# Optimization experiments

Hardware: AMD Instinct MI355X
Metric: run time of the kernel (lower is better)

Reference implementation:

```python
import jax, jax.numpy as jnp
import numpy as np

N_NODES = 100000
N_EDGES = 1600000
D_FEAT = 64  # node feature dim; apply_func indim = 2*D_FEAT, outdim = D_FEAT


def setup_inputs() -> dict:
    key = jax.random.key(0)
    k1, k2, k3, k4 = jax.random.split(key, 4)
    h = jax.random.normal(k1, (N_NODES, D_FEAT), dtype=jnp.float32)
    src = jax.random.randint(k2, (N_EDGES,), 0, N_NODES, dtype=jnp.int32)
    dst = jax.random.randint(k3, (N_EDGES,), 0, N_NODES, dtype=jnp.int32)
    W = jax.random.normal(k4, (D_FEAT, 2 * D_FEAT), dtype=jnp.float32) / jnp.sqrt(2.0 * D_FEAT)
    b = jnp.zeros((D_FEAT,), dtype=jnp.float32)
    return {"h": h, "W": W, "b": b, "src": src, "dst": dst}


def reference(h, W, b, src, dst):
    n = h.shape[0]
    # message passing: gather source features, mean-reduce per destination node
    msgs = h[src]                                                # [E, D]
    summed = jax.ops.segment_sum(msgs, dst, num_segments=n)     # [N, D]
    deg = jax.ops.segment_sum(jnp.ones(dst.shape, h.dtype), dst, num_segments=n)  # [N]
    c = summed / jnp.maximum(deg, 1.0)[:, None]                 # mean aggregate
    # update: concat(h, c) -> linear -> L2 normalize -> relu
    bundle = jnp.concatenate([h, c], axis=1) @ W.T + b           # [N, D]
    norm = jnp.linalg.norm(bundle, axis=1, keepdims=True)
    bundle = bundle / jnp.maximum(norm, 1e-12)                   # F.normalize(p=2, dim=1)
    new_h = jax.nn.relu(bundle)
    # DGL update_all only touches nodes that received messages
    h_upd = jnp.where(deg[:, None] > 0, new_h, h)
    # residual (indim == outdim)
    return h + h_upd
```

## Files before the change

### kernel.cpp

```cpp
#include <hip/hip_runtime.h>

#define DF 64
#define ELLK 32
#define NB 1024
#define BSTR 1792
#define NPB 98

typedef __attribute__((ext_vector_type(8))) short bf16x8;
typedef __attribute__((ext_vector_type(4))) float f32x4;

__device__ __forceinline__ unsigned short bf16rne(float f) {
    unsigned u = __float_as_uint(f);
    unsigned r = u + 0x7fffu + ((u >> 16) & 1u);
    return (unsigned short)(r >> 16);
}
__device__ __forceinline__ float b2f(unsigned short u) {
    return __uint_as_float((unsigned)u << 16);
}

__global__ __launch_bounds__(256) void conv_zero(
    const float* __restrict__ h, unsigned short* __restrict__ hbs,
    int* __restrict__ gcur, int* __restrict__ ovfcnt, int N)
{
    int tid = blockIdx.x * 256 + threadIdx.x;
    if (tid < NB) gcur[tid] = 0;
    if (tid == NB) *ovfcnt = 0;
    if (tid < (N + 1) * 8) {
        int n = tid >> 3, f8 = tid & 7;
        unsigned short* op = &hbs[(size_t)n * DF + f8 * 8];
        if (n == N) {
            ushort4 z = {0, 0, 0, 0};
            *(ushort4*)op = z; *(ushort4*)(op + 4) = z;
        } else {
            const float* hp = &h[(size_t)n * DF + f8 * 8];
            float4 v0 = *(const float4*)hp;
            float4 v1 = *(const float4*)(hp + 4);
            ushort4 o0, o1;
            o0.x = bf16rne(v0.x); o0.y = bf16rne(v0.y); o0.z = bf16rne(v0.z); o0.w = bf16rne(v0.w);
            o1.x = bf16rne(v1.x); o1.y = bf16rne(v1.y); o1.z = bf16rne(v1.z); o1.w = bf16rne(v1.w);
            *(ushort4*)op = o0;
            *(ushort4*)(op + 4) = o1;
        }
    }
}

#define EPT 13
__global__ __launch_bounds__(256) void bin_edges(
    const int* __restrict__ src, const int* __restrict__ dst,
    int* __restrict__ gcur, unsigned* __restrict__ pairs,
    int* __restrict__ ovf, int* __restrict__ ovfcnt, int ovfcap, int E, int N)
{
    __shared__ unsigned hist[NB];
    __shared__ unsigned base_s[NB];
    int t = threadIdx.x;
    for (int i = t; i < NB; i += 256) hist[i] = 0;
    __syncthreads();

    int e0 = blockIdx.x * (EPT * 256);
    unsigned pk[EPT];
    #pragma unroll
    for (int k = 0; k < EPT; ++k) {
        int e = e0 + k * 256 + t;
        pk[k] = 0xFFFFFFFFu;
        if (e < E) {
            int d = dst[e];
            unsigned bkt = (unsigned)(((unsigned long long)d * NB) / (unsigned)N);
            unsigned r = atomicAdd(&hist[bkt], 1u);
            pk[k] = (r << 10) | bkt;
        }
    }
    __syncthreads();
    int rot = (blockIdx.x * 67) & (NB - 1);
    for (int i = t; i < NB; i += 256) {
        int ii = (i + rot) & (NB - 1);
        unsigned hv = hist[ii];
        if (hv) base_s[ii] = (unsigned)atomicAdd(&gcur[ii], (int)hv);
    }
    __syncthreads();

    #pragma unroll
    for (int k = 0; k < EPT; ++k) {
        if (pk[k] != 0xFFFFFFFFu) {
            int e = e0 + k * 256 + t;
            int d = dst[e], s = src[e];
            unsigned bkt = pk[k] & (NB - 1u);
            unsigned pos = base_s[bkt] + (pk[k] >> 10);
            if (pos < BSTR) {
                int lo = (int)(((long long)bkt * N + NB - 1) / NB);
                pairs[(size_t)bkt * BSTR + pos] = ((unsigned)(d - lo) << 17) | (unsigned)s;
            } else {
                int p = atomicAdd(ovfcnt, 1);
                if (p < ovfcap) { ovf[2 * p] = d; ovf[2 * p + 1] = s; }
            }
        }
    }
}

__global__ __launch_bounds__(512) void build_gather(
    const unsigned* __restrict__ pairs, const int* __restrict__ gcur,
    const unsigned short* __restrict__ hbs,
    int* __restrict__ cnt, unsigned short* __restrict__ csum,
    int* __restrict__ ovf, int* __restrict__ ovfcnt, int ovfcap, int N)
{
    __shared__ int ell_l[NPB * ELLK];
    __shared__ int cnt_l[NPB];
    int b = blockIdx.x, t = threadIdx.x;
    int lo = (int)(((long long)b * N + NB - 1) / NB);
    int hi = (int)(((long long)(b + 1) * N + NB - 1) / NB);
    if (hi > N) hi = N;
    int nn = hi - lo;
    for (int i = t; i < nn; i += 512) cnt_l[i] = 0;
    __syncthreads();

    int count = gcur[b]; if (count > BSTR) count = BSTR;
    const unsigned* pb = &pairs[(size_t)b * BSTR];
    for (int i = t; i < count; i += 512) {
        unsigned p = pb[i];
        int ld = (int)(p >> 17);
        int s  = (int)(p & 131071u);
        int slot = atomicAdd(&cnt_l[ld], 1);
        if (slot < ELLK) {
            ell_l[ld * ELLK + (((slot & 7) << 2) | (slot >> 3))] = s;
        } else {
            int q = atomicAdd(ovfcnt, 1);
            if (q < ovfcap) { ovf[2 * q] = lo + ld; ovf[2 * q + 1] = s; }
        }
    }
    __syncthreads();

    const int lane = t & 63, wv = t >> 6;
    const int ew = lane >> 3;
    const int f8 = lane & 7;

    for (int ld = wv; ld < nn; ld += 8) {
        int cv = cnt_l[ld];
        int m = cv < ELLK ? cv : ELLK;
        int ms = __builtin_amdgcn_readfirstlane(m);
        int4 pv = ((const int4*)&ell_l[ld * ELLK])[ew];

        int i0 = (ew     < m) ? pv.x : N;
        int i1 = (ew + 8 < m) ? pv.y : N;
        bf16x8 v0 = *(const bf16x8*)&hbs[(size_t)i0 * DF + f8 * 8];
        bf16x8 v1 = *(const bf16x8*)&hbs[(size_t)i1 * DF + f8 * 8];
        bf16x8 v2 = {0,0,0,0,0,0,0,0};
        bf16x8 v3 = {0,0,0,0,0,0,0,0};
        if (ms > 16) {
            int i2 = (ew + 16 < m) ? pv.z : N;
            v2 = *(const bf16x8*)&hbs[(size_t)i2 * DF + f8 * 8];
            if (ms > 24) {
                int i3 = (ew + 24 < m) ? pv.w : N;
                v3 = *(const bf16x8*)&hbs[(size_t)i3 * DF + f8 * 8];
            }
        }

        float a[8];
        #pragma unroll
        for (int j = 0; j < 8; ++j)
            a[j] = (b2f((unsigned short)v0[j]) + b2f((unsigned short)v1[j]))
                 + (b2f((unsigned short)v2[j]) + b2f((unsigned short)v3[j]));

        #pragma unroll
        for (int msk = 8; msk <= 32; msk <<= 1) {
            #pragma unroll
            for (int j = 0; j < 8; ++j) a[j] += __shfl_xor(a[j], msk);
        }

        if (ew == 0) {
            bf16x8 o;
            #pragma unroll
            for (int j = 0; j < 8; ++j) o[j] = (short)bf16rne(a[j]);
            *(bf16x8*)&csum[(size_t)(lo + ld) * DF + f8 * 8] = o;
        }
    }

    for (int i = t; i < nn; i += 512) {
        int c = cnt_l[i];
        cnt[lo + i] = c < ELLK ? c : ELLK;
    }
}

__global__ __launch_bounds__(256) void sage_update_mfma(
    const float* __restrict__ h, const float* __restrict__ W,
    const float* __restrict__ b, const int* __restrict__ cnt,
    const unsigned short* __restrict__ hbs,
    const unsigned short* __restrict__ csum,
    const int* __restrict__ ovf, const int* __restrict__ ovfcnt,
    int ovfcap, float* __restrict__ out, int N)
{
    const int lane = threadIdx.x & 63;
    const int wave = threadIdx.x >> 6;
    const int c = lane & 15;
    const int q = lane >> 4;

    bf16x8 bf[4][4];
    #pragma unroll
    for (int nt = 0; nt < 4; ++nt) {
        #pragma unroll
        for (int kt = 0; kt < 4; ++kt) {
            const float* wp = &W[(size_t)(nt * 16 + c) * 128 + kt * 32 + q * 8];
            float4 w0 = *(const float4*)wp;
            float4 w1 = *(const float4*)(wp + 4);
            bf16x8 f;
            f[0] = (short)bf16rne(w0.x); f[1] = (short)bf16rne(w0.y);
            f[2] = (short)bf16rne(w0.z); f[3] = (short)bf16rne(w0.w);
            f[4] = (short)bf16rne(w1.x); f[5] = (short)bf16rne(w1.y);
            f[6] = (short)bf16rne(w1.z); f[7] = (short)bf16rne(w1.w);
            bf[nt][kt] = f;
        }
    }
    float bias[4];
    #pragma unroll
    for (int nt = 0; nt < 4; ++nt) bias[nt] = b[nt * 16 + c];

    int oc = *ovfcnt; if (oc > ovfcap) oc = ovfcap;

    int gwave = blockIdx.x * 4 + wave;
    int nwave = gridDim.x * 4;
    int ntiles = (N + 15) >> 4;

    for (int tile = gwave; tile < ntiles; tile += nwave) {
        int n0 = tile << 4;
        int nm = n0 + c;
        int nmc = nm < N ? nm : N - 1;
        int deg = cnt[nmc];
        int extra = 0;
        if (oc > 0) {
            for (int t = 0; t < oc; ++t)
                if (ovf[2 * t] == nm) extra++;
        }
        int dtot = deg + extra;
        float inv = 1.0f / fmaxf((float)dtot, 1.0f);

        bf16x8 a0 = *(const bf16x8*)&hbs[(size_t)nmc * DF + q * 8];
        bf16x8 a1 = *(const bf16x8*)&hbs[(size_t)nmc * DF + 32 + q * 8];
        bf16x8 a2, a3;
        #pragma unroll
        for (int kc = 0; kc < 2; ++kc) {
            bf16x8 u = *(const bf16x8*)&csum[(size_t)nmc * DF + kc * 32 + q * 8];
            float e[8];
            #pragma unroll
            for (int i = 0; i < 8; ++i) e[i] = b2f((unsigned short)u[i]);
            if (oc > 0) {
                for (int t = 0; t < oc; ++t) {
                    if (ovf[2 * t] == nm) {
                        bf16x8 hu = *(const bf16x8*)&hbs[(size_t)ovf[2 * t + 1] * DF + kc * 32 + q * 8];
                        #pragma unroll
                        for (int i = 0; i < 8; ++i) e[i] += b2f((unsigned short)hu[i]);
                    }
                }
            }
            bf16x8 f;
            #pragma unroll
            for (int i = 0; i < 8; ++i) f[i] = (short)bf16rne(e[i] * inv);
            if (kc == 0) a2 = f; else a3 = f;
        }

        f32x4 acc0 = {bias[0], bias[0], bias[0], bias[0]};
        f32x4 acc1 = {bias[1], bias[1], bias[1], bias[1]};
        f32x4 acc2 = {bias[2], bias[2], bias[2], bias[2]};
        f32x4 acc3 = {bias[3], bias[3], bias[3], bias[3]};
        acc0 = __builtin_amdgcn_mfma_f32_16x16x32_bf16(a0, bf[0][0], acc0, 0, 0, 0);
        acc0 = __builtin_amdgcn_mfma_f32_16x16x32_bf16(a1, bf[0][1], acc0, 0, 0, 0);
        acc0 = __builtin_amdgcn_mfma_f32_16x16x32_bf16(a2, bf[0][2], acc0, 0, 0, 0);
        acc0 = __builtin_amdgcn_mfma_f32_16x16x32_bf16(a3, bf[0][3], acc0, 0, 0, 0);
        acc1 = __builtin_amdgcn_mfma_f32_16x16x32_bf16(a0, bf[1][0], acc1, 0, 0, 0);
        acc1 = __builtin_amdgcn_mfma_f32_16x16x32_bf16(a1, bf[1][1], acc1, 0, 0, 0);
        acc1 = __builtin_amdgcn_mfma_f32_16x16x32_bf16(a2, bf[1][2], acc1, 0, 0, 0);
        acc1 = __builtin_amdgcn_mfma_f32_16x16x32_bf16(a3, bf[1][3], acc1, 0, 0, 0);
        acc2 = __builtin_amdgcn_mfma_f32_16x16x32_bf16(a0, bf[2][0], acc2, 0, 0, 0);
        acc2 = __builtin_amdgcn_mfma_f32_16x16x32_bf16(a1, bf[2][1], acc2, 0, 0, 0);
        acc2 = __builtin_amdgcn_mfma_f32_16x16x32_bf16(a2, bf[2][2], acc2, 0, 0, 0);
        acc2 = __builtin_amdgcn_mfma_f32_16x16x32_bf16(a3, bf[2][3], acc2, 0, 0, 0);
        acc3 = __builtin_amdgcn_mfma_f32_16x16x32_bf16(a0, bf[3][0], acc3, 0, 0, 0);
        acc3 = __builtin_amdgcn_mfma_f32_16x16x32_bf16(a1, bf[3][1], acc3, 0, 0, 0);
        acc3 = __builtin_amdgcn_mfma_f32_16x16x32_bf16(a2, bf[3][2], acc3, 0, 0, 0);
        acc3 = __builtin_amdgcn_mfma_f32_16x16x32_bf16(a3, bf[3][3], acc3, 0, 0, 0);

        float ss[4];
        #pragma unroll
        for (int r = 0; r < 4; ++r)
            ss[r] = acc0[r] * acc0[r] + acc1[r] * acc1[r]
                  + acc2[r] * acc2[r] + acc3[r] * acc3[r];
        #pragma unroll
        for (int msk = 1; msk <= 8; msk <<= 1) {
            ss[0] += __shfl_xor(ss[0], msk);
            ss[1] += __shfl_xor(ss[1], msk);
            ss[2] += __shfl_xor(ss[2], msk);
            ss[3] += __shfl_xor(ss[3], msk);
        }
        #pragma unroll
        for (int r = 0; r < 4; ++r) {
            int nr = n0 + q * 4 + r;
            int dr = __shfl(deg + extra, q * 4 + r);
            if (nr < N) {
                float rin = 1.0f / fmaxf(sqrtf(ss[r]), 1e-12f);
                const float* hp = &h[(size_t)nr * DF + c];
                float hv0 = hp[0], hv1 = hp[16], hv2 = hp[32], hv3 = hp[48];
                bool up = dr > 0;
                float o0 = hv0 + (up ? fmaxf(acc0[r] * rin, 0.f) : hv0);
                float o1 = hv1 + (up ? fmaxf(acc1[r] * rin, 0.f) : hv1);
                float o2 = hv2 + (up ? fmaxf(acc2[r] * rin, 0.f) : hv2);
                float o3 = hv3 + (up ? fmaxf(acc3[r] * rin, 0.f) : hv3);
                float* op = &out[(size_t)nr * DF + c];
                op[0] = o0; op[16] = o1; op[32] = o2; op[48] = o3;
            }
        }
    }
}

extern "C" void kernel_launch(void* const* d_in, const int* in_sizes, int n_in,
                              void* d_out, int out_size, void* d_ws, size_t ws_size,
                              hipStream_t stream) {
    const float* h   = (const float*)d_in[0];
    const float* W   = (const float*)d_in[1];
    const float* b   = (const float*)d_in[2];
    const int*   src = (const int*)d_in[3];
    const int*   dst = (const int*)d_in[4];
    float* out = (float*)d_out;

    const int N = in_sizes[0] / DF;
    const int E = in_sizes[3];

    int* cnt    = (int*)d_ws;
    int* ovfcnt = cnt + N;
    int* gcur   = cnt + ((N + 31) & ~15);
    unsigned short* hbs  = (unsigned short*)(gcur + ((NB + 15) & ~15));
    unsigned short* csum = hbs + (((size_t)(N + 1) * DF + 15) & ~(size_t)15);
    unsigned* pairs = (unsigned*)(csum + (((size_t)N * DF + 15) & ~(size_t)15));
    int* ovf    = (int*)(pairs + (size_t)NB * BSTR);
    size_t used = (size_t)((char*)ovf - (char*)d_ws);
    int ovfcap  = (ws_size > used + 64) ? (int)((ws_size - used) / 8 - 4) : 0;

    conv_zero<<<((N + 1) * 8 + 255) / 256, 256, 0, stream>>>(h, hbs, gcur, ovfcnt, N);

    bin_edges<<<(E + EPT * 256 - 1) / (EPT * 256), 256, 0, stream>>>(
        src, dst, gcur, pairs, ovf, ovfcnt, ovfcap, E, N);

    build_gather<<<NB, 512, 0, stream>>>(
        pairs, gcur, hbs, cnt, csum, ovf, ovfcnt, ovfcap, N);

    sage_update_mfma<<<512, 256, 0, stream>>>(
        h, W, b, cnt, hbs, csum, ovf, ovfcnt, ovfcap, out, N);
}
```

Baseline: 207.5 us.

## Use coarser 256-bucket binning with four gather blocks per bucket

```diff
diff --git a/kernel.cpp b/kernel.cpp
--- a/kernel.cpp
+++ b/kernel.cpp
@@ -2,8 +2,9 @@
 
 #define DF 64
 #define ELLK 32
-#define NB 1024
-#define BSTR 1792
+#define NBB 256
+#define GQ 4
+#define BSTR 7168
 #define NPB 98
 
 typedef __attribute__((ext_vector_type(8))) short bf16x8;
@@ -23,8 +24,8 @@
     int* __restrict__ gcur, int* __restrict__ ovfcnt, int N)
 {
     int tid = blockIdx.x * 256 + threadIdx.x;
-    if (tid < NB) gcur[tid] = 0;
-    if (tid == NB) *ovfcnt = 0;
+    if (tid < NBB) gcur[tid] = 0;
+    if (tid == NBB) *ovfcnt = 0;
     if (tid < (N + 1) * 8) {
         int n = tid >> 3, f8 = tid & 7;
         unsigned short* op = &hbs[(size_t)n * DF + f8 * 8];
@@ -50,10 +51,10 @@
     int* __restrict__ gcur, unsigned* __restrict__ pairs,
     int* __restrict__ ovf, int* __restrict__ ovfcnt, int ovfcap, int E, int N)
 {
-    __shared__ unsigned hist[NB];
-    __shared__ unsigned base_s[NB];
+    __shared__ unsigned hist[NBB];
+    __shared__ unsigned base_s[NBB];
     int t = threadIdx.x;
-    for (int i = t; i < NB; i += 256) hist[i] = 0;
+    if (t < NBB) hist[t] = 0;
     __syncthreads();
 
     int e0 = blockIdx.x * (EPT * 256);
@@ -64,15 +65,15 @@
         pk[k] = 0xFFFFFFFFu;
         if (e < E) {
             int d = dst[e];
-            unsigned bkt = (unsigned)(((unsigned long long)d * NB) / (unsigned)N);
+            unsigned bkt = (unsigned)(((unsigned long long)d * NBB) / (unsigned)N);
             unsigned r = atomicAdd(&hist[bkt], 1u);
-            pk[k] = (r << 10) | bkt;
-        }
-    }
-    __syncthreads();
-    int rot = (blockIdx.x * 67) & (NB - 1);
-    for (int i = t; i < NB; i += 256) {
-        int ii = (i + rot) & (NB - 1);
+            pk[k] = (r << 8) | bkt;
+        }
+    }
+    __syncthreads();
+    int rot = (blockIdx.x * 67) & (NBB - 1);
+    if (t < NBB) {
+        int ii = (t + rot) & (NBB - 1);
         unsigned hv = hist[ii];
         if (hv) base_s[ii] = (unsigned)atomicAdd(&gcur[ii], (int)hv);
     }
@@ -83,10 +84,10 @@
         if (pk[k] != 0xFFFFFFFFu) {
             int e = e0 + k * 256 + t;
             int d = dst[e], s = src[e];
-            unsigned bkt = pk[k] & (NB - 1u);
-            unsigned pos = base_s[bkt] + (pk[k] >> 10);
+            unsigned bkt = pk[k] & (NBB - 1u);
+            unsigned pos = base_s[bkt] + (pk[k] >> 8);
             if (pos < BSTR) {
-                int lo = (int)(((long long)bkt * N + NB - 1) / NB);
+                int lo = (int)(((long long)bkt * N + NBB - 1) / NBB);
                 pairs[(size_t)bkt * BSTR + pos] = ((unsigned)(d - lo) << 17) | (unsigned)s;
             } else {
                 int p = atomicAdd(ovfcnt, 1);
@@ -104,26 +105,34 @@
 {
     __shared__ int ell_l[NPB * ELLK];
     __shared__ int cnt_l[NPB];
-    int b = blockIdx.x, t = threadIdx.x;
-    int lo = (int)(((long long)b * N + NB - 1) / NB);
-    int hi = (int)(((long long)(b + 1) * N + NB - 1) / NB);
-    if (hi > N) hi = N;
-    int nn = hi - lo;
-    for (int i = t; i < nn; i += 512) cnt_l[i] = 0;
+    int b = blockIdx.x >> 2, qt = blockIdx.x & 3;
+    int t = threadIdx.x;
+    int lo_b = (int)(((long long)b * N + NBB - 1) / NBB);
+    int hi_b = (int)(((long long)(b + 1) * N + NBB - 1) / NBB);
+    if (hi_b > N) hi_b = N;
+    int nn_b = hi_b - lo_b;
+    int q0 = qt * NPB;
+    int qn = nn_b - q0; if (qn > NPB) qn = NPB;
+    if (qn <= 0) return;
+    int nbase = lo_b + q0;
+
+    for (int i = t; i < qn; i += 512) cnt_l[i] = 0;
     __syncthreads();
 
     int count = gcur[b]; if (count > BSTR) count = BSTR;
     const unsigned* pb = &pairs[(size_t)b * BSTR];
     for (int i = t; i < count; i += 512) {
         unsigned p = pb[i];
-        int ld = (int)(p >> 17);
-        int s  = (int)(p & 131071u);
-        int slot = atomicAdd(&cnt_l[ld], 1);
-        if (slot < ELLK) {
-            ell_l[ld * ELLK + (((slot & 7) << 2) | (slot >> 3))] = s;
-        } else {
-            int q = atomicAdd(ovfcnt, 1);
-            if (q < ovfcap) { ovf[2 * q] = lo + ld; ovf[2 * q + 1] = s; }
+        int ld = (int)(p >> 17) - q0;
+        if ((unsigned)ld < (unsigned)qn) {
+            int s = (int)(p & 131071u);
+            int slot = atomicAdd(&cnt_l[ld], 1);
+            if (slot < ELLK) {
+                ell_l[ld * ELLK + (((slot & 7) << 2) | (slot >> 3))] = s;
+            } else {
+                int q = atomicAdd(ovfcnt, 1);
+                if (q < ovfcap) { ovf[2 * q] = nbase + ld; ovf[2 * q + 1] = s; }
+            }
         }
     }
     __syncthreads();
@@ -132,7 +141,7 @@
     const int ew = lane >> 3;
     const int f8 = lane & 7;
 
-    for (int ld = wv; ld < nn; ld += 8) {
+    for (int ld = wv; ld < qn; ld += 8) {
         int cv = cnt_l[ld];
         int m = cv < ELLK ? cv : ELLK;
         int ms = __builtin_amdgcn_readfirstlane(m);
@@ -169,13 +178,13 @@
             bf16x8 o;
             #pragma unroll
             for (int j = 0; j < 8; ++j) o[j] = (short)bf16rne(a[j]);
-            *(bf16x8*)&csum[(size_t)(lo + ld) * DF + f8 * 8] = o;
-        }
-    }
-
-    for (int i = t; i < nn; i += 512) {
+            *(bf16x8*)&csum[(size_t)(nbase + ld) * DF + f8 * 8] = o;
+        }
+    }
+
+    for (int i = t; i < qn; i += 512) {
         int c = cnt_l[i];
-        cnt[lo + i] = c < ELLK ? c : ELLK;
+        cnt[nbase + i] = c < ELLK ? c : ELLK;
     }
 }
 
@@ -324,10 +333,10 @@
     int* cnt    = (int*)d_ws;
     int* ovfcnt = cnt + N;
     int* gcur   = cnt + ((N + 31) & ~15);
-    unsigned short* hbs  = (unsigned short*)(gcur + ((NB + 15) & ~15));
+    unsigned short* hbs  = (unsigned short*)(gcur + ((NBB + 15) & ~15));
     unsigned short* csum = hbs + (((size_t)(N + 1) * DF + 15) & ~(size_t)15);
     unsigned* pairs = (unsigned*)(csum + (((size_t)N * DF + 15) & ~(size_t)15));
-    int* ovf    = (int*)(pairs + (size_t)NB * BSTR);
+    int* ovf    = (int*)(pairs + (size_t)NBB * BSTR);
     size_t used = (size_t)((char*)ovf - (char*)d_ws);
     int ovfcap  = (ws_size > used + 64) ? (int)((ws_size - used) / 8 - 4) : 0;
 
@@ -336,7 +345,7 @@
     bin_edges<<<(E + EPT * 256 - 1) / (EPT * 256), 256, 0, stream>>>(
         src, dst, gcur, pairs, ovf, ovfcnt, ovfcap, E, N);
 
-    build_gather<<<NB, 512, 0, stream>>>(
+    build_gather<<<NBB * GQ, 512, 0, stream>>>(
         pairs, gcur, hbs, cnt, csum, ovf, ovfcnt, ovfcap, N);
 
     sage_update_mfma<<<512, 256, 0, stream>>>(
```

New measurement: 200.0 us. 3.6% less time.

## Scatter edges into a global ELL with atomics and fuse the gather into the update

Applied to the files above, without the earlier changes.

```diff
diff --git a/kernel.cpp b/kernel.cpp
--- a/kernel.cpp
+++ b/kernel.cpp
@@ -2,9 +2,8 @@
 
 #define DF 64
 #define ELLK 32
-#define NB 1024
-#define BSTR 1792
-#define NPB 98
+#define WIN 64
+#define CSTR 72
 
 typedef __attribute__((ext_vector_type(8))) short bf16x8;
 typedef __attribute__((ext_vector_type(4))) float f32x4;
@@ -18,13 +17,14 @@
     return __uint_as_float((unsigned)u << 16);
 }
 
-__global__ __launch_bounds__(256) void conv_zero(
-    const float* __restrict__ h, unsigned short* __restrict__ hbs,
-    int* __restrict__ gcur, int* __restrict__ ovfcnt, int N)
+__global__ __launch_bounds__(512) void conv_scatter(
+    const float* __restrict__ h, const int* __restrict__ src,
+    const int* __restrict__ dst, unsigned short* __restrict__ hbs,
+    int* __restrict__ cnt, int* __restrict__ ell,
+    int* __restrict__ ovf, int* __restrict__ ovfcnt, int ovfcap, int N, int E)
 {
-    int tid = blockIdx.x * 256 + threadIdx.x;
-    if (tid < NB) gcur[tid] = 0;
-    if (tid == NB) *ovfcnt = 0;
+    int tid = blockIdx.x * 512 + threadIdx.x;
+
     if (tid < (N + 1) * 8) {
         int n = tid >> 3, f8 = tid & 7;
         unsigned short* op = &hbs[(size_t)n * DF + f8 * 8];
@@ -42,156 +42,80 @@
             *(ushort4*)(op + 4) = o1;
         }
     }
-}
-
-#define EPT 13
-__global__ __launch_bounds__(256) void bin_edges(
-    const int* __restrict__ src, const int* __restrict__ dst,
-    int* __restrict__ gcur, unsigned* __restrict__ pairs,
-    int* __restrict__ ovf, int* __restrict__ ovfcnt, int ovfcap, int E, int N)
-{
-    __shared__ unsigned hist[NB];
-    __shared__ unsigned base_s[NB];
-    int t = threadIdx.x;
-    for (int i = t; i < NB; i += 256) hist[i] = 0;
-    __syncthreads();
-
-    int e0 = blockIdx.x * (EPT * 256);
-    unsigned pk[EPT];
-    #pragma unroll
-    for (int k = 0; k < EPT; ++k) {
-        int e = e0 + k * 256 + t;
-        pk[k] = 0xFFFFFFFFu;
-        if (e < E) {
-            int d = dst[e];
-            unsigned bkt = (unsigned)(((unsigned long long)d * NB) / (unsigned)N);
-            unsigned r = atomicAdd(&hist[bkt], 1u);
-            pk[k] = (r << 10) | bkt;
-        }
-    }
-    __syncthreads();
-    int rot = (blockIdx.x * 67) & (NB - 1);
-    for (int i = t; i < NB; i += 256) {
-        int ii = (i + rot) & (NB - 1);
-        unsigned hv = hist[ii];
-        if (hv) base_s[ii] = (unsigned)atomicAdd(&gcur[ii], (int)hv);
-    }
-    __syncthreads();
-
-    #pragma unroll
-    for (int k = 0; k < EPT; ++k) {
-        if (pk[k] != 0xFFFFFFFFu) {
-            int e = e0 + k * 256 + t;
-            int d = dst[e], s = src[e];
-            unsigned bkt = pk[k] & (NB - 1u);
-            unsigned pos = base_s[bkt] + (pk[k] >> 10);
-            if (pos < BSTR) {
-                int lo = (int)(((long long)bkt * N + NB - 1) / NB);
-                pairs[(size_t)bkt * BSTR + pos] = ((unsigned)(d - lo) << 17) | (unsigned)s;
-            } else {
-                int p = atomicAdd(ovfcnt, 1);
-                if (p < ovfcap) { ovf[2 * p] = d; ovf[2 * p + 1] = s; }
-            }
-        }
-    }
-}
-
-__global__ __launch_bounds__(512) void build_gather(
-    const unsigned* __restrict__ pairs, const int* __restrict__ gcur,
-    const unsigned short* __restrict__ hbs,
-    int* __restrict__ cnt, unsigned short* __restrict__ csum,
-    int* __restrict__ ovf, int* __restrict__ ovfcnt, int ovfcap, int N)
-{
-    __shared__ int ell_l[NPB * ELLK];
-    __shared__ int cnt_l[NPB];
-    int b = blockIdx.x, t = threadIdx.x;
-    int lo = (int)(((long long)b * N + NB - 1) / NB);
-    int hi = (int)(((long long)(b + 1) * N + NB - 1) / NB);
-    if (hi > N) hi = N;
-    int nn = hi - lo;
-    for (int i = t; i < nn; i += 512) cnt_l[i] = 0;
-    __syncthreads();
-
-    int count = gcur[b]; if (count > BSTR) count = BSTR;
-    const unsigned* pb = &pairs[(size_t)b * BSTR];
-    for (int i = t; i < count; i += 512) {
-        unsigned p = pb[i];
-        int ld = (int)(p >> 17);
-        int s  = (int)(p & 131071u);
-        int slot = atomicAdd(&cnt_l[ld], 1);
+
+    int stride = gridDim.x * 512;
+    for (int e = tid; e < E; e += stride) {
+        int d = dst[e], s = src[e];
+        int slot = atomicAdd(&cnt[d], 1);
         if (slot < ELLK) {
-            ell_l[ld * ELLK + (((slot & 7) << 2) | (slot >> 3))] = s;
+            ell[(size_t)d * ELLK + (((slot & 7) << 2) | (slot >> 3))] = s;
         } else {
-            int q = atomicAdd(ovfcnt, 1);
-            if (q < ovfcap) { ovf[2 * q] = lo + ld; ovf[2 * q + 1] = s; }
-        }
-    }
-    __syncthreads();
-
-    const int lane = t & 63, wv = t >> 6;
-    const int ew = lane >> 3;
-    const int f8 = lane & 7;
-
-    for (int ld = wv; ld < nn; ld += 8) {
-        int cv = cnt_l[ld];
-        int m = cv < ELLK ? cv : ELLK;
-        int ms = __builtin_amdgcn_readfirstlane(m);
-        int4 pv = ((const int4*)&ell_l[ld * ELLK])[ew];
-
-        int i0 = (ew     < m) ? pv.x : N;
-        int i1 = (ew + 8 < m) ? pv.y : N;
-        bf16x8 v0 = *(const bf16x8*)&hbs[(size_t)i0 * DF + f8 * 8];
-        bf16x8 v1 = *(const bf16x8*)&hbs[(size_t)i1 * DF + f8 * 8];
-        bf16x8 v2 = {0,0,0,0,0,0,0,0};
-        bf16x8 v3 = {0,0,0,0,0,0,0,0};
-        if (ms > 16) {
-            int i2 = (ew + 16 < m) ? pv.z : N;
-            v2 = *(const bf16x8*)&hbs[(size_t)i2 * DF + f8 * 8];
-            if (ms > 24) {
-                int i3 = (ew + 24 < m) ? pv.w : N;
-                v3 = *(const bf16x8*)&hbs[(size_t)i3 * DF + f8 * 8];
-            }
-        }
-
-        float a[8];
-        #pragma unroll
-        for (int j = 0; j < 8; ++j)
-            a[j] = (b2f((unsigned short)v0[j]) + b2f((unsigned short)v1[j]))
-                 + (b2f((unsigned short)v2[j]) + b2f((unsigned short)v3[j]));
-
-        #pragma unroll
-        for (int msk = 8; msk <= 32; msk <<= 1) {
-            #pragma unroll
-            for (int j = 0; j < 8; ++j) a[j] += __shfl_xor(a[j], msk);
-        }
-
-        if (ew == 0) {
-            bf16x8 o;
-            #pragma unroll
-            for (int j = 0; j < 8; ++j) o[j] = (short)bf16rne(a[j]);
-            *(bf16x8*)&csum[(size_t)(lo + ld) * DF + f8 * 8] = o;
-        }
-    }
-
-    for (int i = t; i < nn; i += 512) {
-        int c = cnt_l[i];
-        cnt[lo + i] = c < ELLK ? c : ELLK;
-    }
-}
-
-__global__ __launch_bounds__(256) void sage_update_mfma(
-    const float* __restrict__ h, const float* __restrict__ W,
-    const float* __restrict__ b, const int* __restrict__ cnt,
-    const unsigned short* __restrict__ hbs,
-    const unsigned short* __restrict__ csum,
+            int p = atomicAdd(ovfcnt, 1);
+            if (p < ovfcap) { ovf[2 * p] = d; ovf[2 * p + 1] = s; }
+        }
+    }
+}
+
+__global__ __launch_bounds__(256, 4) void gather_update(
+    const unsigned short* __restrict__ hbs, const int* __restrict__ cnt,
+    const int* __restrict__ ell, const float* __restrict__ h,
+    const float* __restrict__ W, const float* __restrict__ b,
     const int* __restrict__ ovf, const int* __restrict__ ovfcnt,
     int ovfcap, float* __restrict__ out, int N)
 {
-    const int lane = threadIdx.x & 63;
-    const int wave = threadIdx.x >> 6;
-    const int c = lane & 15;
-    const int q = lane >> 4;
-
+    __shared__ unsigned short csB[WIN * CSTR];
+    const int t = threadIdx.x, lane = t & 63, wv = t >> 6;
+    const int base = blockIdx.x * WIN;
+
+    const int ew = lane >> 3;
+    const int f8 = lane & 7;
+    for (int i = 0; i < WIN / 4; ++i) {
+        int ld = wv + 4 * i;
+        int n = base + ld;
+        if (n < N) {
+            int cv = cnt[n];
+            int m = cv < ELLK ? cv : ELLK;
+            int ms = __builtin_amdgcn_readfirstlane(m);
+            int4 pv = *(const int4*)&ell[(size_t)n * ELLK + 4 * ew];
+
+            int i0 = (ew     < m) ? pv.x : N;
+            int i1 = (ew + 8 < m) ? pv.y : N;
+            bf16x8 v0 = *(const bf16x8*)&hbs[(size_t)i0 * DF + f8 * 8];
+            bf16x8 v1 = *(const bf16x8*)&hbs[(size_t)i1 * DF + f8 * 8];
+            bf16x8 v2 = {0,0,0,0,0,0,0,0};
+            bf16x8 v3 = {0,0,0,0,0,0,0,0};
+            if (ms > 16) {
+                int i2 = (ew + 16 < m) ? pv.z : N;
+                v2 = *(const bf16x8*)&hbs[(size_t)i2 * DF + f8 * 8];
+                if (ms > 24) {
+                    int i3 = (ew + 24 < m) ? pv.w : N;
+                    v3 = *(const bf16x8*)&hbs[(size_t)i3 * DF + f8 * 8];
+                }
+            }
+
+            float a[8];
+            #pragma unroll
+            for (int j = 0; j < 8; ++j)
+                a[j] = (b2f((unsigned short)v0[j]) + b2f((unsigned short)v1[j]))
+                     + (b2f((unsigned short)v2[j]) + b2f((unsigned short)v3[j]));
+            #pragma unroll
+            for (int msk = 8; msk <= 32; msk <<= 1) {
+                #pragma unroll
+                for (int j = 0; j < 8; ++j) a[j] += __shfl_xor(a[j], msk);
+            }
+            if (ew == 0) {
+                bf16x8 o;
+                #pragma unroll
+                for (int j = 0; j < 8; ++j) o[j] = (short)bf16rne(a[j]);
+                *(bf16x8*)&csB[ld * CSTR + f8 * 8] = o;
+            }
+        } else if (ew == 0) {
+            bf16x8 z = {0,0,0,0,0,0,0,0};
+            *(bf16x8*)&csB[ld * CSTR + f8 * 8] = z;
+        }
+    }
+
+    const int c = lane & 15, q = lane >> 4;
     bf16x8 bf[4][4];
     #pragma unroll
     for (int nt = 0; nt < 4; ++nt) {
@@ -214,96 +138,86 @@
 
     int oc = *ovfcnt; if (oc > ovfcap) oc = ovfcap;
 
-    int gwave = blockIdx.x * 4 + wave;
-    int nwave = gridDim.x * 4;
-    int ntiles = (N + 15) >> 4;
-
-    for (int tile = gwave; tile < ntiles; tile += nwave) {
-        int n0 = tile << 4;
-        int nm = n0 + c;
-        int nmc = nm < N ? nm : N - 1;
-        int deg = cnt[nmc];
-        int extra = 0;
+    __syncthreads();
+
+    int wn0 = wv * 16;
+    int nm = base + wn0 + c;
+    int nmc = nm < N ? nm : N - 1;
+    int dtot = cnt[nmc];
+    float inv = 1.0f / fmaxf((float)dtot, 1.0f);
+
+    bf16x8 a0 = *(const bf16x8*)&hbs[(size_t)nmc * DF + q * 8];
+    bf16x8 a1 = *(const bf16x8*)&hbs[(size_t)nmc * DF + 32 + q * 8];
+    bf16x8 a2, a3;
+    #pragma unroll
+    for (int kc = 0; kc < 2; ++kc) {
+        bf16x8 u = *(const bf16x8*)&csB[(wn0 + c) * CSTR + kc * 32 + q * 8];
+        float e[8];
+        #pragma unroll
+        for (int i = 0; i < 8; ++i) e[i] = b2f((unsigned short)u[i]);
         if (oc > 0) {
-            for (int t = 0; t < oc; ++t)
-                if (ovf[2 * t] == nm) extra++;
-        }
-        int dtot = deg + extra;
-        float inv = 1.0f / fmaxf((float)dtot, 1.0f);
-
-        bf16x8 a0 = *(const bf16x8*)&hbs[(size_t)nmc * DF + q * 8];
-        bf16x8 a1 = *(const bf16x8*)&hbs[(size_t)nmc * DF + 32 + q * 8];
-        bf16x8 a2, a3;
+            for (int t2 = 0; t2 < oc; ++t2) {
+                if (ovf[2 * t2] == nm) {
+                    bf16x8 hu = *(const bf16x8*)&hbs[(size_t)ovf[2 * t2 + 1] * DF + kc * 32 + q * 8];
+                    #pragma unroll
+                    for (int i = 0; i < 8; ++i) e[i] += b2f((unsigned short)hu[i]);
+                }
+            }
+        }
+        bf16x8 f;
         #pragma unroll
-        for (int kc = 0; kc < 2; ++kc) {
-            bf16x8 u = *(const bf16x8*)&csum[(size_t)nmc * DF + kc * 32 + q * 8];
-            float e[8];
-            #pragma unroll
-            for (int i = 0; i < 8; ++i) e[i] = b2f((unsigned short)u[i]);
-            if (oc > 0) {
-                for (int t = 0; t < oc; ++t) {
-                    if (ovf[2 * t] == nm) {
-                        bf16x8 hu = *(const bf16x8*)&hbs[(size_t)ovf[2 * t + 1] * DF + kc * 32 + q * 8];
-                        #pragma unroll
-                        for (int i = 0; i < 8; ++i) e[i] += b2f((unsigned short)hu[i]);
-                    }
-                }
-            }
-            bf16x8 f;
-            #pragma unroll
-            for (int i = 0; i < 8; ++i) f[i] = (short)bf16rne(e[i] * inv);
-            if (kc == 0) a2 = f; else a3 = f;
-        }
-
-        f32x4 acc0 = {bias[0], bias[0], bias[0], bias[0]};
-        f32x4 acc1 = {bias[1], bias[1], bias[1], bias[1]};
-        f32x4 acc2 = {bias[2], bias[2], bias[2], bias[2]};
-        f32x4 acc3 = {bias[3], bias[3], bias[3], bias[3]};
-        acc0 = __builtin_amdgcn_mfma_f32_16x16x32_bf16(a0, bf[0][0], acc0, 0, 0, 0);
-        acc0 = __builtin_amdgcn_mfma_f32_16x16x32_bf16(a1, bf[0][1], acc0, 0, 0, 0);
-        acc0 = __builtin_amdgcn_mfma_f32_16x16x32_bf16(a2, bf[0][2], acc0, 0, 0, 0);
-        acc0 = __builtin_amdgcn_mfma_f32_16x16x32_bf16(a3, bf[0][3], acc0, 0, 0, 0);
-        acc1 = __builtin_amdgcn_mfma_f32_16x16x32_bf16(a0, bf[1][0], acc1, 0, 0, 0);
-        acc1 = __builtin_amdgcn_mfma_f32_16x16x32_bf16(a1, bf[1][1], acc1, 0, 0, 0);
-        acc1 = __builtin_amdgcn_mfma_f32_16x16x32_bf16(a2, bf[1][2], acc1, 0, 0, 0);
-        acc1 = __builtin_amdgcn_mfma_f32_16x16x32_bf16(a3, bf[1][3], acc1, 0, 0, 0);
-        acc2 = __builtin_amdgcn_mfma_f32_16x16x32_bf16(a0, bf[2][0], acc2, 0, 0, 0);
-        acc2 = __builtin_amdgcn_mfma_f32_16x16x32_bf16(a1, bf[2][1], acc2, 0, 0, 0);
-        acc2 = __builtin_amdgcn_mfma_f32_16x16x32_bf16(a2, bf[2][2], acc2, 0, 0, 0);
-        acc2 = __builtin_amdgcn_mfma_f32_16x16x32_bf16(a3, bf[2][3], acc2, 0, 0, 0);
-        acc3 = __builtin_amdgcn_mfma_f32_16x16x32_bf16(a0, bf[3][0], acc3, 0, 0, 0);
-        acc3 = __builtin_amdgcn_mfma_f32_16x16x32_bf16(a1, bf[3][1], acc3, 0, 0, 0);
-        acc3 = __builtin_amdgcn_mfma_f32_16x16x32_bf16(a2, bf[3][2], acc3, 0, 0, 0);
-        acc3 = __builtin_amdgcn_mfma_f32_16x16x32_bf16(a3, bf[3][3], acc3, 0, 0, 0);
-
-        float ss[4];
-        #pragma unroll
-        for (int r = 0; r < 4; ++r)
-            ss[r] = acc0[r] * acc0[r] + acc1[r] * acc1[r]
-                  + acc2[r] * acc2[r] + acc3[r] * acc3[r];
-        #pragma unroll
-        for (int msk = 1; msk <= 8; msk <<= 1) {
-            ss[0] += __shfl_xor(ss[0], msk);
-            ss[1] += __shfl_xor(ss[1], msk);
-            ss[2] += __shfl_xor(ss[2], msk);
-            ss[3] += __shfl_xor(ss[3], msk);
-        }
-        #pragma unroll
-        for (int r = 0; r < 4; ++r) {
-            int nr = n0 + q * 4 + r;
-            int dr = __shfl(deg + extra, q * 4 + r);
-            if (nr < N) {
-                float rin = 1.0f / fmaxf(sqrtf(ss[r]), 1e-12f);
-                const float* hp = &h[(size_t)nr * DF + c];
-                float hv0 = hp[0], hv1 = hp[16], hv2 = hp[32], hv3 = hp[48];
-                bool up = dr > 0;
-                float o0 = hv0 + (up ? fmaxf(acc0[r] * rin, 0.f) : hv0);
-                float o1 = hv1 + (up ? fmaxf(acc1[r] * rin, 0.f) : hv1);
-                float o2 = hv2 + (up ? fmaxf(acc2[r] * rin, 0.f) : hv2);
-                float o3 = hv3 + (up ? fmaxf(acc3[r] * rin, 0.f) : hv3);
-                float* op = &out[(size_t)nr * DF + c];
-                op[0] = o0; op[16] = o1; op[32] = o2; op[48] = o3;
-            }
+        for (int i = 0; i < 8; ++i) f[i] = (short)bf16rne(e[i] * inv);
+        if (kc == 0) a2 = f; else a3 = f;
+    }
+
+    f32x4 acc0 = {bias[0], bias[0], bias[0], bias[0]};
+    f32x4 acc1 = {bias[1], bias[1], bias[1], bias[1]};
+    f32x4 acc2 = {bias[2], bias[2], bias[2], bias[2]};
+    f32x4 acc3 = {bias[3], bias[3], bias[3], bias[3]};
+    acc0 = __builtin_amdgcn_mfma_f32_16x16x32_bf16(a0, bf[0][0], acc0, 0, 0, 0);
+    acc0 = __builtin_amdgcn_mfma_f32_16x16x32_bf16(a1, bf[0][1], acc0, 0, 0, 0);
+    acc0 = __builtin_amdgcn_mfma_f32_16x16x32_bf16(a2, bf[0][2], acc0, 0, 0, 0);
+    acc0 = __builtin_amdgcn_mfma_f32_16x16x32_bf16(a3, bf[0][3], acc0, 0, 0, 0);
+    acc1 = __builtin_amdgcn_mfma_f32_16x16x32_bf16(a0, bf[1][0], acc1, 0, 0, 0);
+    acc1 = __builtin_amdgcn_mfma_f32_16x16x32_bf16(a1, bf[1][1], acc1, 0, 0, 0);
+    acc1 = __builtin_amdgcn_mfma_f32_16x16x32_bf16(a2, bf[1][2], acc1, 0, 0, 0);
+    acc1 = __builtin_amdgcn_mfma_f32_16x16x32_bf16(a3, bf[1][3], acc1, 0, 0, 0);
+    acc2 = __builtin_amdgcn_mfma_f32_16x16x32_bf16(a0, bf[2][0], acc2, 0, 0, 0);
+    acc2 = __builtin_amdgcn_mfma_f32_16x16x32_bf16(a1, bf[2][1], acc2, 0, 0, 0);
+    acc2 = __builtin_amdgcn_mfma_f32_16x16x32_bf16(a2, bf[2][2], acc2, 0, 0, 0);
+    acc2 = __builtin_amdgcn_mfma_f32_16x16x32_bf16(a3, bf[2][3], acc2, 0, 0, 0);
+    acc3 = __builtin_amdgcn_mfma_f32_16x16x32_bf16(a0, bf[3][0], acc3, 0, 0, 0);
+    acc3 = __builtin_amdgcn_mfma_f32_16x16x32_bf16(a1, bf[3][1], acc3, 0, 0, 0);
+    acc3 = __builtin_amdgcn_mfma_f32_16x16x32_bf16(a2, bf[3][2], acc3, 0, 0, 0);
+    acc3 = __builtin_amdgcn_mfma_f32_16x16x32_bf16(a3, bf[3][3], acc3, 0, 0, 0);
+
+    float ss[4];
+    #pragma unroll
+    for (int r = 0; r < 4; ++r)
+        ss[r] = acc0[r] * acc0[r] + acc1[r] * acc1[r]
+              + acc2[r] * acc2[r] + acc3[r] * acc3[r];
+    #pragma unroll
+    for (int msk = 1; msk <= 8; msk <<= 1) {
+        ss[0] += __shfl_xor(ss[0], msk);
+        ss[1] += __shfl_xor(ss[1], msk);
+        ss[2] += __shfl_xor(ss[2], msk);
+        ss[3] += __shfl_xor(ss[3], msk);
+    }
+    #pragma unroll
+    for (int r = 0; r < 4; ++r) {
+        int nr = base + wn0 + q * 4 + r;
+        int dr = __shfl(dtot, q * 4 + r);
+        if (nr < N) {
+            float rin = 1.0f / fmaxf(sqrtf(ss[r]), 1e-12f);
+            const float* hp = &h[(size_t)nr * DF + c];
+            float hv0 = hp[0], hv1 = hp[16], hv2 = hp[32], hv3 = hp[48];
+            bool up = dr > 0;
+            float o0 = hv0 + (up ? fmaxf(acc0[r] * rin, 0.f) : hv0);
+            float o1 = hv1 + (up ? fmaxf(acc1[r] * rin, 0.f) : hv1);
+            float o2 = hv2 + (up ? fmaxf(acc2[r] * rin, 0.f) : hv2);
+            float o3 = hv3 + (up ? fmaxf(acc3[r] * rin, 0.f) : hv3);
+            float* op = &out[(size_t)nr * DF + c];
+            op[0] = o0; op[16] = o1; op[32] = o2; op[48] = o3;
         }
     }
 }
@@ -323,22 +237,17 @@
 
     int* cnt    = (int*)d_ws;
     int* ovfcnt = cnt + N;
-    int* gcur   = cnt + ((N + 31) & ~15);
-    unsigned short* hbs  = (unsigned short*)(gcur + ((NB + 15) & ~15));
-    unsigned short* csum = hbs + (((size_t)(N + 1) * DF + 15) & ~(size_t)15);
-    unsigned* pairs = (unsigned*)(csum + (((size_t)N * DF + 15) & ~(size_t)15));
-    int* ovf    = (int*)(pairs + (size_t)NB * BSTR);
+    int* ell    = cnt + ((N + 1 + 15) & ~15);
+    unsigned short* hbs = (unsigned short*)(ell + (size_t)N * ELLK);
+    int* ovf    = (int*)(hbs + (size_t)(N + 1) * DF);
     size_t used = (size_t)((char*)ovf - (char*)d_ws);
     int ovfcap  = (ws_size > used + 64) ? (int)((ws_size - used) / 8 - 4) : 0;
 
-    conv_zero<<<((N + 1) * 8 + 255) / 256, 256, 0, stream>>>(h, hbs, gcur, ovfcnt, N);
-
-    bin_edges<<<(E + EPT * 256 - 1) / (EPT * 256), 256, 0, stream>>>(
-        src, dst, gcur, pairs, ovf, ovfcnt, ovfcap, E, N);
-
-    build_gather<<<NB, 512, 0, stream>>>(
-        pairs, gcur, hbs, cnt, csum, ovf, ovfcnt, ovfcap, N);
-
-    sage_update_mfma<<<512, 256, 0, stream>>>(
-        h, W, b, cnt, hbs, csum, ovf, ovfcnt, ovfcap, out, N);
-}
+    hipMemsetAsync(cnt, 0, (size_t)(N + 1) * sizeof(int), stream);
+
+    conv_scatter<<<2048, 512, 0, stream>>>(
+        h, src, dst, hbs, cnt, ell, ovf, ovfcnt, ovfcap, N, E);
+
+    gather_update<<<(N + WIN - 1) / WIN, 256, 0, stream>>>(
+        hbs, cnt, ell, h, W, b, ovf, ovfcnt, ovfcap, out, N);
+}
```

Result: slower. 307.8 us (+48.3%).
